# Performance work log

Measured on AMD Instinct MI355X. Metric: run time of the kernel, lower is better.

Reference implementation:

```python
import jax, jax.numpy as jnp
import numpy as np

N_GRAPHS = 8192
NODES_PER_GRAPH = 62
IN_CH = 4
HID = 64
NUM_CLASSES = 3
DEG = 8
N = N_GRAPHS * NODES_PER_GRAPH        # 507904 total nodes
E = N * DEG                            # 4063232 edges
BN_EPS = 1e-5


def setup_inputs() -> dict:
    key = jax.random.key(0)
    ks = jax.random.split(key, 24)

    def lin_w(k, i, o):
        return (jax.random.normal(k, (i, o), jnp.float32) / np.float32(np.sqrt(i)))

    inp = {
        "x": jax.random.normal(ks[0], (N, IN_CH), jnp.float32),
        "edge_src": jax.random.randint(ks[1], (E,), 0, N, dtype=jnp.int32),
        "edge_dst": jax.random.randint(ks[2], (E,), 0, N, dtype=jnp.int32),
        "num_graphs": N_GRAPHS,
        # conv1 MLP: Linear(4,64) -> ReLU -> Linear(64,64)
        "W1a": lin_w(ks[3], IN_CH, HID), "b1a": jnp.zeros((HID,), jnp.float32),
        "W1b": lin_w(ks[4], HID, HID),   "b1b": jnp.zeros((HID,), jnp.float32),
        "g1": jnp.ones((HID,), jnp.float32), "be1": jnp.zeros((HID,), jnp.float32),
        # conv2 MLP
        "W2a": lin_w(ks[5], HID, HID), "b2a": jnp.zeros((HID,), jnp.float32),
        "W2b": lin_w(ks[6], HID, HID), "b2b": jnp.zeros((HID,), jnp.float32),
        "g2": jnp.ones((HID,), jnp.float32), "be2": jnp.zeros((HID,), jnp.float32),
        # conv3 MLP
        "W3a": lin_w(ks[7], HID, HID), "b3a": jnp.zeros((HID,), jnp.float32),
        "W3b": lin_w(ks[8], HID, HID), "b3b": jnp.zeros((HID,), jnp.float32),
        "g3": jnp.ones((HID,), jnp.float32), "be3": jnp.zeros((HID,), jnp.float32),
        # final classifier fc2 (fc1 is unused in the original forward)
        "Wfc": lin_w(ks[9], HID, NUM_CLASSES), "bfc": jnp.zeros((NUM_CLASSES,), jnp.float32),
    }
    return inp


def _gin_conv(x, src, dst, Wa, ba, Wb, bb):
    # GINConv with eps=0: mlp(x_i + sum_{j->i} x_j)
    agg = jax.ops.segment_sum(x[src], dst, num_segments=N)
    h = x + agg
    return jnp.maximum(h @ Wa + ba, 0.0) @ Wb + bb


def _bn(h, g, b):
    # BatchNorm1d with batch statistics (training-mode math)
    m = h.mean(axis=0)
    v = h.var(axis=0)
    return (h - m) * jax.lax.rsqrt(v + BN_EPS) * g + b


def reference(x, edge_src, edge_dst, num_graphs,
              W1a, b1a, W1b, b1b, g1, be1,
              W2a, b2a, W2b, b2b, g2, be2,
              W3a, b3a, W3b, b3b, g3, be3,
              Wfc, bfc):
    h = _bn(jnp.maximum(_gin_conv(x, edge_src, edge_dst, W1a, b1a, W1b, b1b), 0.0), g1, be1)
    h = _bn(jnp.maximum(_gin_conv(h, edge_src, edge_dst, W2a, b2a, W2b, b2b), 0.0), g2, be2)
    h = _bn(jnp.maximum(_gin_conv(h, edge_src, edge_dst, W3a, b3a, W3b, b3b), 0.0), g3, be3)
    h = h.reshape(num_graphs, -1, HID).sum(axis=1)   # sum-pool nodes per graph
    # dropout is identity in eval mode
    return h @ Wfc + bfc
```

## Files before the change

kernel.cpp:

```cpp
#include <hip/hip_runtime.h>
#include <hip/hip_bf16.h>

#define NN   507904
#define NE   4063232
#define NG   8192
#define NPG  62
#define NBLKM 992

#define NB    248
#define BRNG  2048
#define BCAP  17152
#define PBCAP 31744
#define P3BLK 992
#define CSRSZ (NB * PBCAP)

#define OFF_R     0
#define OFF_AGGBF (OFF_R + NN * 64)
#define OFF_CSR   (OFF_AGGBF + NN * 32 + 32)
#define OFF_OC    (OFF_CSR + CSRSZ)
#define OFF_BCUR  (OFF_OC + 2 * NN)
#define OFF_PART  (OFF_BCUR + 256)
#define OFF_WTB   (OFF_PART + NBLKM * 128)
#define OFF_SS    (OFF_WTB + 11264)

#define WB_W1B 0
#define WB_W2A 4096
#define WB_W2B 8192
#define WB_W3A 12288
#define WB_W3B 16384
#define WB_W1A 20480

typedef __attribute__((ext_vector_type(8))) short short8;
typedef __attribute__((ext_vector_type(4))) float f32x4;
typedef unsigned short ushort_t;

__device__ __forceinline__ ushort_t f2bf_bits(float f) {
  union { float f; unsigned u; } x; x.f = f;
  unsigned r = x.u + 0x7FFF + ((x.u >> 16) & 1);
  return (ushort_t)(r >> 16);
}
__device__ __forceinline__ float bfu(ushort_t u) {
  union { unsigned i; float f; } x; x.i = ((unsigned)u) << 16; return x.f;
}

__global__ __launch_bounds__(256) void prep_weights(
    const float* __restrict__ w1a, const float* __restrict__ w1b,
    const float* __restrict__ w2a, const float* __restrict__ w2b,
    const float* __restrict__ w3a, const float* __restrict__ w3b,
    ushort_t* __restrict__ wtb, int* __restrict__ bcur,
    unsigned* __restrict__ sent1, unsigned* __restrict__ sent2) {
  int b = blockIdx.x, tid = threadIdx.x;
  if (b == 0) {
    ushort_t* d = wtb + WB_W1A;
    for (int i = tid; i < 2048; i += 256) {
      int n = i >> 5, k = i & 31;
      d[i] = (k < 4) ? f2bf_bits(w1a[k * 64 + n]) : (ushort_t)0;
    }
  } else if (b == 6) {
    bcur[tid] = 0;
    if (tid < 32) { sent1[tid] = 0; sent2[tid] = 0; }
  } else {
    const float* s; ushort_t* d;
    switch (b) {
      case 1: s = w1b; d = wtb + WB_W1B; break;
      case 2: s = w2a; d = wtb + WB_W2A; break;
      case 3: s = w2b; d = wtb + WB_W2B; break;
      case 4: s = w3a; d = wtb + WB_W3A; break;
      default: s = w3b; d = wtb + WB_W3B; break;
    }
    for (int i = tid; i < 4096; i += 256) {
      int k = i >> 6, n = i & 63;
      d[n * 64 + k] = f2bf_bits(s[i]);
    }
  }
}

__global__ __launch_bounds__(256) void p3_bin(
    const int* __restrict__ src, const int* __restrict__ dst,
    int* __restrict__ bcur, uint2* __restrict__ recs) {
  __shared__ int histo[256];
  __shared__ int scan_s[256];
  __shared__ int base_s[256];
  __shared__ int cur_s[256];
  __shared__ uint2 buf[4096];
  const int tid = threadIdx.x;
  const int e0 = blockIdx.x * 4096;

  histo[tid] = 0;
  __syncthreads();

  int d_[16], s_[16];
#pragma unroll
  for (int k = 0; k < 16; ++k) {
    int e = e0 + k * 256 + tid;
    d_[k] = dst[e]; s_[k] = src[e];
    atomicAdd(&histo[d_[k] >> 11], 1);
  }
  __syncthreads();

  int v = histo[tid];
  scan_s[tid] = v; __syncthreads();
  for (int s = 1; s < 256; s <<= 1) {
    int add = (tid >= s) ? scan_s[tid - s] : 0;
    __syncthreads();
    scan_s[tid] += add;
    __syncthreads();
  }
  int excl = scan_s[tid] - v;
  if (tid < NB) base_s[tid] = atomicAdd(&bcur[tid], v);
  cur_s[tid] = excl;
  histo[tid] = excl;
  __syncthreads();

#pragma unroll
  for (int k = 0; k < 16; ++k) {
    int b = d_[k] >> 11;
    int p = atomicAdd(&cur_s[b], 1);
    uint2 r; r.x = (unsigned)d_[k]; r.y = (unsigned)s_[k];
    buf[p] = r;
  }
  __syncthreads();

  for (int i = tid; i < 4096; i += 256) {
    uint2 r = buf[i];
    int b = (int)(r.x >> 11);
    int g = base_s[b] + (i - histo[b]);
    if (g < BCAP) recs[(size_t)b * BCAP + g] = r;
  }
}

__global__ __launch_bounds__(1024) void p4_build(
    const uint2* __restrict__ recs, const int* __restrict__ bcur,
    int* __restrict__ csr, int2* __restrict__ oc) {
  __shared__ int lcnt[2048];
  __shared__ int pscan[1024];
  __shared__ int sstart[2048];
  __shared__ int scur[2048];
  const int b = blockIdx.x, tid = threadIdx.x;
  int m = bcur[b]; if (m > BCAP) m = BCAP;
  const int cbase = b * PBCAP;
  const int nbase = b << 11;
  const uint2* rp = recs + (size_t)b * BCAP;

  lcnt[tid] = 0; lcnt[1024 + tid] = 0;
  __syncthreads();
  for (int i = tid; i < m; i += 1024)
    atomicAdd(&lcnt[rp[i].x & (BRNG - 1)], 1);
  __syncthreads();

  int a0 = lcnt[2 * tid], a1 = lcnt[2 * tid + 1];
  int p0 = (a0 + 7) & ~7, p1 = (a1 + 7) & ~7;
  int ps = p0 + p1;
  pscan[tid] = ps; __syncthreads();
  for (int s = 1; s < 1024; s <<= 1) {
    int add = (tid >= s) ? pscan[tid - s] : 0;
    __syncthreads();
    pscan[tid] += add;
    __syncthreads();
  }
  int e0 = pscan[tid] - ps;
  sstart[2 * tid] = e0;          scur[2 * tid] = e0;
  sstart[2 * tid + 1] = e0 + p0; scur[2 * tid + 1] = e0 + p0;
  __syncthreads();

  {
    int2 r0; r0.x = cbase + sstart[tid];        r0.y = lcnt[tid];
    int2 r1; r1.x = cbase + sstart[1024 + tid]; r1.y = lcnt[1024 + tid];
    oc[nbase + tid] = r0;
    oc[nbase + 1024 + tid] = r1;
  }
  __syncthreads();

  for (int i = tid; i < m; i += 1024) {
    uint2 r = rp[i];
    int p = atomicAdd(&scur[r.x & (BRNG - 1)], 1);
    csr[cbase + p] = (int)r.y;
  }
  __syncthreads();

#pragma unroll
  for (int k = 0; k < 2; ++k) {
    int i = k * 1024 + tid;
    int st = sstart[i], d = lcnt[i], p = (d + 7) & ~7;
    for (int q = d; q < p; ++q) csr[cbase + st + q] = NN;
  }
}

__global__ __launch_bounds__(256) void gather1(
    const float4* __restrict__ x, const int* __restrict__ csr,
    const int2* __restrict__ oc, float4* __restrict__ tout) {
  int n = blockIdx.x * 256 + threadIdx.x;
  float4 a = x[n];
  int2 oc_ = oc[n];
  int off = oc_.x, deg = oc_.y;
  const int* cp = csr + off;
  int j = 0;
  for (; j + 4 <= deg; j += 4) {
    int s0 = cp[j], s1 = cp[j + 1], s2 = cp[j + 2], s3 = cp[j + 3];
    float4 v0 = x[s0], v1 = x[s1], v2 = x[s2], v3 = x[s3];
    a.x += v0.x + v1.x + v2.x + v3.x;
    a.y += v0.y + v1.y + v2.y + v3.y;
    a.z += v0.z + v1.z + v2.z + v3.z;
    a.w += v0.w + v1.w + v2.w + v3.w;
  }
  for (; j < deg; ++j) {
    float4 v = x[cp[j]];
    a.x += v.x; a.y += v.y; a.z += v.z; a.w += v.w;
  }
  tout[n] = a;
}

template <bool L1, bool BFOUT>
__global__ __launch_bounds__(256) void mlp_mfma(
    const void* __restrict__ tin,
    const ushort_t* __restrict__ WaTb,
    const float* __restrict__ ba,
    const ushort_t* __restrict__ WbTb,
    const float* __restrict__ bb,
    float* __restrict__ routf, ushort_t* __restrict__ routb,
    float* __restrict__ part) {
  __shared__ __align__(16) ushort_t zt[4096];
  __shared__ float red[512];
  const int tid = threadIdx.x;
  const int wave = tid >> 6, lane = tid & 63;
  const int col = lane & 15, quad = lane >> 4;

  short8 bWa1[4];
  short8 bWa[2][4];
  short8 bWb[2][4];
#pragma unroll
  for (int nt = 0; nt < 4; ++nt) {
    if (L1) {
      bWa1[nt] = *(const short8*)(WaTb + (nt * 16 + col) * 32 + quad * 8);
    } else {
#pragma unroll
      for (int k0 = 0; k0 < 2; ++k0)
        bWa[k0][nt] = *(const short8*)(WaTb + (nt * 16 + col) * 64 + k0 * 32 + quad * 8);
    }
#pragma unroll
    for (int k0 = 0; k0 < 2; ++k0)
      bWb[k0][nt] = *(const short8*)(WbTb + (nt * 16 + col) * 64 + k0 * 32 + quad * 8);
  }
  float ba_n[4], bb_n[4];
#pragma unroll
  for (int nt = 0; nt < 4; ++nt) {
    ba_n[nt] = ba[nt * 16 + col];
    bb_n[nt] = bb[nt * 16 + col];
  }

  const int wbase = wave * 1024;
  float scol[4] = {0, 0, 0, 0}, qcol[4] = {0, 0, 0, 0};

  for (int it = 0; it < 8; ++it) {
    const int tile = blockIdx.x * 512 + it * 64 + wave * 16;

    f32x4 acc1[4];
#pragma unroll
    for (int nt = 0; nt < 4; ++nt) acc1[nt] = (f32x4){0.f, 0.f, 0.f, 0.f};

    if constexpr (L1) {
      float4 t4 = ((const float4*)tin)[tile + col];
      short8 az = {0, 0, 0, 0, 0, 0, 0, 0};
      if (quad == 0) {
        az[0] = (short)f2bf_bits(t4.x);
        az[1] = (short)f2bf_bits(t4.y);
        az[2] = (short)f2bf_bits(t4.z);
        az[3] = (short)f2bf_bits(t4.w);
      }
#pragma unroll
      for (int nt = 0; nt < 4; ++nt)
        acc1[nt] = __builtin_amdgcn_mfma_f32_16x16x32_bf16(az, bWa1[nt], acc1[nt], 0, 0, 0);
    } else {
      const ushort_t* tb = (const ushort_t*)tin;
      short8 a0 = *(const short8*)(tb + (size_t)(tile + col) * 64 + quad * 8);
      short8 a1 = *(const short8*)(tb + (size_t)(tile + col) * 64 + 32 + quad * 8);
#pragma unroll
      for (int nt = 0; nt < 4; ++nt) {
        acc1[nt] = __builtin_amdgcn_mfma_f32_16x16x32_bf16(a0, bWa[0][nt], acc1[nt], 0, 0, 0);
        acc1[nt] = __builtin_amdgcn_mfma_f32_16x16x32_bf16(a1, bWa[1][nt], acc1[nt], 0, 0, 0);
      }
    }

#pragma unroll
    for (int nt = 0; nt < 4; ++nt) {
      int oblk = nt * 2 + (col >> 3);
#pragma unroll
      for (int r = 0; r < 4; ++r) {
        int row = quad * 4 + r;
        float z = fmaxf(acc1[nt][r] + ba_n[nt], 0.0f);
        zt[wbase + row * 64 + (((oblk ^ (row & 7)) << 3) | (col & 7))] = f2bf_bits(z);
      }
    }
    short8 az0 = *(const short8*)&zt[wbase + col * 64 + ((quad ^ (col & 7)) << 3)];
    short8 az1 = *(const short8*)&zt[wbase + col * 64 + (((4 + quad) ^ (col & 7)) << 3)];

    f32x4 acc2[4];
#pragma unroll
    for (int nt = 0; nt < 4; ++nt) acc2[nt] = (f32x4){0.f, 0.f, 0.f, 0.f};
#pragma unroll
    for (int nt = 0; nt < 4; ++nt) {
      acc2[nt] = __builtin_amdgcn_mfma_f32_16x16x32_bf16(az0, bWb[0][nt], acc2[nt], 0, 0, 0);
      acc2[nt] = __builtin_amdgcn_mfma_f32_16x16x32_bf16(az1, bWb[1][nt], acc2[nt], 0, 0, 0);
    }
#pragma unroll
    for (int nt = 0; nt < 4; ++nt) {
#pragma unroll
      for (int r = 0; r < 4; ++r) {
        int row = tile + quad * 4 + r;
        float v = fmaxf(acc2[nt][r] + bb_n[nt], 0.0f);
        if (BFOUT) routb[(size_t)row * 64 + nt * 16 + col] = f2bf_bits(v);
        else       routf[(size_t)row * 64 + nt * 16 + col] = v;
        scol[nt] += v; qcol[nt] += v * v;
      }
    }
  }

#pragma unroll
  for (int nt = 0; nt < 4; ++nt) {
    float s = scol[nt], q = qcol[nt];
    s += __shfl_xor(s, 16); s += __shfl_xor(s, 32);
    q += __shfl_xor(q, 16); q += __shfl_xor(q, 32);
    if (quad == 0) {
      red[wave * 128 + nt * 16 + col] = s;
      red[wave * 128 + 64 + nt * 16 + col] = q;
    }
  }
  __syncthreads();
  if (tid < 128)
    part[blockIdx.x * 128 + tid] =
        red[tid] + red[128 + tid] + red[256 + tid] + red[384 + tid];
}

template <bool BFOUT>
__global__ __launch_bounds__(256) void mlp_fused(
    const ushort_t* __restrict__ h,
    const int* __restrict__ csr, const int2* __restrict__ oc,
    const float* __restrict__ ss,
    const ushort_t* __restrict__ WaTb,
    const float* __restrict__ ba,
    const ushort_t* __restrict__ WbTb,
    const float* __restrict__ bb,
    float* __restrict__ routf, ushort_t* __restrict__ routb,
    float* __restrict__ part) {
  __shared__ __align__(16) ushort_t zt[4096];
  __shared__ float red[512];
  __shared__ float ssl[128];
  const int tid = threadIdx.x;
  const int wave = tid >> 6, lane = tid & 63;
  const int col = lane & 15, quad = lane >> 4;
  if (tid < 128) ssl[tid] = ss[tid];

  short8 bWa[2][4], bWb[2][4];
#pragma unroll
  for (int nt = 0; nt < 4; ++nt) {
#pragma unroll
    for (int k0 = 0; k0 < 2; ++k0) {
      bWa[k0][nt] = *(const short8*)(WaTb + (nt * 16 + col) * 64 + k0 * 32 + quad * 8);
      bWb[k0][nt] = *(const short8*)(WbTb + (nt * 16 + col) * 64 + k0 * 32 + quad * 8);
    }
  }
  float ba_n[4], bb_n[4];
#pragma unroll
  for (int nt = 0; nt < 4; ++nt) {
    ba_n[nt] = ba[nt * 16 + col];
    bb_n[nt] = bb[nt * 16 + col];
  }
  __syncthreads();

  const float* scA = ssl + quad * 8;
  const float* scB = ssl + 32 + quad * 8;
  const float* sfA = ssl + 64 + quad * 8;
  const float* sfB = ssl + 96 + quad * 8;

  const int wbase = wave * 1024;
  float scol[4] = {0, 0, 0, 0}, qcol[4] = {0, 0, 0, 0};

  for (int it = 0; it < 8; ++it) {
    const int tile = blockIdx.x * 512 + it * 64 + wave * 16;
    const int row = tile + col;
    const int2 o = oc[row];

    const ushort_t* hp = h + (size_t)(unsigned)row * 64u + quad * 8;
    short8 sl0 = *(const short8*)hp;
    short8 sl1 = *(const short8*)(hp + 32);
    float accA[8], accB[8];
#pragma unroll
    for (int e = 0; e < 8; ++e) {
      accA[e] = bfu((ushort_t)sl0[e]);
      accB[e] = bfu((ushort_t)sl1[e]);
    }

    const int chunks = (o.y + 7) >> 3;
    for (int c = 0; c < chunks; ++c) {
      const int* cp = csr + o.x + (c << 3);
      int4 i0 = *(const int4*)cp;
      int4 i1 = *(const int4*)(cp + 4);
      int idx[8] = {i0.x, i0.y, i0.z, i0.w, i1.x, i1.y, i1.z, i1.w};
#pragma unroll
      for (int j = 0; j < 8; ++j) {
        const ushort_t* p = h + (size_t)(unsigned)idx[j] * 64u + quad * 8;
        short8 l0 = *(const short8*)p;
        short8 l1 = *(const short8*)(p + 32);
#pragma unroll
        for (int e = 0; e < 8; ++e) {
          accA[e] += bfu((ushort_t)l0[e]);
          accB[e] += bfu((ushort_t)l1[e]);
        }
      }
    }

    const float m1 = (float)(o.y + 1);
    short8 a0, a1;
#pragma unroll
    for (int e = 0; e < 8; ++e) {
      a0[e] = (short)f2bf_bits(fmaf(scA[e], accA[e], m1 * sfA[e]));
      a1[e] = (short)f2bf_bits(fmaf(scB[e], accB[e], m1 * sfB[e]));
    }

    f32x4 acc1[4];
#pragma unroll
    for (int nt = 0; nt < 4; ++nt) acc1[nt] = (f32x4){0.f, 0.f, 0.f, 0.f};
#pragma unroll
    for (int nt = 0; nt < 4; ++nt) {
      acc1[nt] = __builtin_amdgcn_mfma_f32_16x16x32_bf16(a0, bWa[0][nt], acc1[nt], 0, 0, 0);
      acc1[nt] = __builtin_amdgcn_mfma_f32_16x16x32_bf16(a1, bWa[1][nt], acc1[nt], 0, 0, 0);
    }

#pragma unroll
    for (int nt = 0; nt < 4; ++nt) {
      int oblk = nt * 2 + (col >> 3);
#pragma unroll
      for (int r = 0; r < 4; ++r) {
        int rw = quad * 4 + r;
        float z = fmaxf(acc1[nt][r] + ba_n[nt], 0.0f);
        zt[wbase + rw * 64 + (((oblk ^ (rw & 7)) << 3) | (col & 7))] = f2bf_bits(z);
      }
    }
    short8 az0 = *(const short8*)&zt[wbase + col * 64 + ((quad ^ (col & 7)) << 3)];
    short8 az1 = *(const short8*)&zt[wbase + col * 64 + (((4 + quad) ^ (col & 7)) << 3)];

    f32x4 acc2[4];
#pragma unroll
    for (int nt = 0; nt < 4; ++nt) acc2[nt] = (f32x4){0.f, 0.f, 0.f, 0.f};
#pragma unroll
    for (int nt = 0; nt < 4; ++nt) {
      acc2[nt] = __builtin_amdgcn_mfma_f32_16x16x32_bf16(az0, bWb[0][nt], acc2[nt], 0, 0, 0);
      acc2[nt] = __builtin_amdgcn_mfma_f32_16x16x32_bf16(az1, bWb[1][nt], acc2[nt], 0, 0, 0);
    }
#pragma unroll
    for (int nt = 0; nt < 4; ++nt) {
#pragma unroll
      for (int r = 0; r < 4; ++r) {
        int rw = tile + quad * 4 + r;
        float v = fmaxf(acc2[nt][r] + bb_n[nt], 0.0f);
        if (BFOUT) routb[(size_t)rw * 64 + nt * 16 + col] = f2bf_bits(v);
        else       routf[(size_t)rw * 64 + nt * 16 + col] = v;
        scol[nt] += v; qcol[nt] += v * v;
      }
    }
  }

#pragma unroll
  for (int nt = 0; nt < 4; ++nt) {
    float s = scol[nt], q = qcol[nt];
    s += __shfl_xor(s, 16); s += __shfl_xor(s, 32);
    q += __shfl_xor(q, 16); q += __shfl_xor(q, 32);
    if (quad == 0) {
      red[wave * 128 + nt * 16 + col] = s;
      red[wave * 128 + 64 + nt * 16 + col] = q;
    }
  }
  __syncthreads();
  if (tid < 128)
    part[blockIdx.x * 128 + tid] =
        red[tid] + red[128 + tid] + red[256 + tid] + red[384 + tid];
}

__global__ __launch_bounds__(256) void reduce_finalize(
    const float* __restrict__ part, const float* __restrict__ gma,
    const float* __restrict__ bta, float* __restrict__ ss) {
  __shared__ double sh[512];
  const int c = blockIdx.x, tid = threadIdx.x;
  double a = 0.0, b = 0.0;
  for (int blk = tid; blk < NBLKM; blk += 256) {
    a += (double)part[blk * 128 + c];
    b += (double)part[blk * 128 + 64 + c];
  }
  sh[tid] = a; sh[256 + tid] = b;
  __syncthreads();
  for (int s = 128; s; s >>= 1) {
    if (tid < s) { sh[tid] += sh[tid + s]; sh[256 + tid] += sh[256 + tid + s]; }
    __syncthreads();
  }
  if (tid == 0) {
    double mean = sh[0] / (double)NN;
    double var = sh[256] / (double)NN - mean * mean;
    double sc = (double)gma[c] / sqrt(var + 1e-5);
    ss[c] = (float)sc;
    ss[64 + c] = (float)((double)bta[c] - mean * sc);
  }
}

__global__ __launch_bounds__(64) void pool_fc(
    const float* __restrict__ r3, const float* __restrict__ ss,
    const float* __restrict__ wfc, const float* __restrict__ bfc,
    float* __restrict__ out) {
  int g = blockIdx.x, c = threadIdx.x;
  const float* base = r3 + (size_t)g * NPG * 64;
  float s = 0.f;
#pragma unroll
  for (int n = 0; n < NPG; ++n) s += base[n * 64 + c];
  float pooled = fmaf(ss[c], s, (float)NPG * ss[64 + c]);
#pragma unroll
  for (int j = 0; j < 3; ++j) {
    float v = pooled * wfc[c * 3 + j];
    for (int m = 32; m; m >>= 1) v += __shfl_xor(v, m);
    if (c == 0) out[g * 3 + j] = v + bfc[j];
  }
}

extern "C" void kernel_launch(void* const* d_in, const int* in_sizes, int n_in,
                              void* d_out, int out_size, void* d_ws, size_t ws_size,
                              hipStream_t stream) {
  const float* x    = (const float*)d_in[0];
  const int*   srcE = (const int*)d_in[1];
  const int*   dstE = (const int*)d_in[2];
  const float* W1a = (const float*)d_in[4],  *b1a = (const float*)d_in[5];
  const float* W1b = (const float*)d_in[6],  *b1b = (const float*)d_in[7];
  const float* g1  = (const float*)d_in[8],  *be1 = (const float*)d_in[9];
  const float* W2a = (const float*)d_in[10], *b2a = (const float*)d_in[11];
  const float* W2b = (const float*)d_in[12], *b2b = (const float*)d_in[13];
  const float* g2  = (const float*)d_in[14], *be2 = (const float*)d_in[15];
  const float* W3a = (const float*)d_in[16], *b3a = (const float*)d_in[17];
  const float* W3b = (const float*)d_in[18], *b3b = (const float*)d_in[19];
  const float* g3  = (const float*)d_in[20], *be3 = (const float*)d_in[21];
  const float* Wfc = (const float*)d_in[22], *bfc = (const float*)d_in[23];

  float* ws = (float*)d_ws;
  ushort_t* Rb     = (ushort_t*)(ws + OFF_R);
  float*    Rf     = ws + OFF_R;
  ushort_t* Ab     = (ushort_t*)(ws + OFF_AGGBF);
  void*     T1     = (void*)(ws + OFF_AGGBF);
  uint2*    RECS   = (uint2*)(ws + OFF_AGGBF);
  int*      CSR    = (int*)(ws + OFF_CSR);
  int2*     OC     = (int2*)(ws + OFF_OC);
  int*      BCUR   = (int*)(ws + OFF_BCUR);
  float*    PART   = ws + OFF_PART;
  ushort_t* WTB    = (ushort_t*)(ws + OFF_WTB);
  float*    SS     = ws + OFF_SS;

  prep_weights<<<7, 256, 0, stream>>>(W1a, W1b, W2a, W2b, W3a, W3b, WTB, BCUR,
                                      (unsigned*)(Rb + (size_t)NN * 64),
                                      (unsigned*)(Ab + (size_t)NN * 64));

  p3_bin<<<P3BLK, 256, 0, stream>>>(srcE, dstE, BCUR, RECS);
  p4_build<<<NB, 1024, 0, stream>>>(RECS, BCUR, CSR, OC);

  gather1<<<NN / 256, 256, 0, stream>>>((const float4*)x, CSR, OC, (float4*)T1);
  mlp_mfma<true, true><<<NBLKM, 256, 0, stream>>>(T1, WTB + WB_W1A, b1a,
                                                  WTB + WB_W1B, b1b,
                                                  nullptr, Rb, PART);
  reduce_finalize<<<64, 256, 0, stream>>>(PART, g1, be1, SS + 0);

  mlp_fused<true><<<NBLKM, 256, 0, stream>>>(Rb, CSR, OC, SS + 0,
                                             WTB + WB_W2A, b2a,
                                             WTB + WB_W2B, b2b,
                                             nullptr, Ab, PART);
  reduce_finalize<<<64, 256, 0, stream>>>(PART, g2, be2, SS + 128);

  mlp_fused<false><<<NBLKM, 256, 0, stream>>>(Ab, CSR, OC, SS + 128,
                                              WTB + WB_W3A, b3a,
                                              WTB + WB_W3B, b3b,
                                              Rf, nullptr, PART);
  reduce_finalize<<<64, 256, 0, stream>>>(PART, g3, be3, SS + 256);

  pool_fc<<<NG, 64, 0, stream>>>(Rf, SS + 256, Wfc, bfc, (float*)d_out);
}
```

Before: 567.8 us.

## Fuse graph sum-pooling into layer-3 MLP and coalesce bf16 output stores

Layer 3 no longer writes its full fp32 activation matrix. Each block accumulates per-graph sums in shared memory with atomics and flushes them to a global per-graph buffer with atomics, and a small fc_out kernel reads these sums. Layer 1 and layer 2 outputs are staged through swizzled LDS so each lane writes 16-byte vectors instead of scattered 2-byte stores. Blocks are halved in size, doubling the grid and the partial-stats count. The goal is to remove the large fp32 write and re-read for pooling and to improve store coalescing, at the cost of shared and global atomic contention.

```diff
diff --git a/kernel.cpp b/kernel.cpp
--- a/kernel.cpp
+++ b/kernel.cpp
@@ -5,7 +5,7 @@
 #define NE   4063232
 #define NG   8192
 #define NPG  62
-#define NBLKM 992
+#define NPBLK 1984
 
 #define NB    248
 #define BRNG  2048
@@ -15,12 +15,13 @@
 #define CSRSZ (NB * PBCAP)
 
 #define OFF_R     0
+#define OFF_GSUM  (OFF_R + NN * 32 + 64)
+#define OFF_PART  (OFF_GSUM + NG * 64)
 #define OFF_AGGBF (OFF_R + NN * 64)
 #define OFF_CSR   (OFF_AGGBF + NN * 32 + 32)
 #define OFF_OC    (OFF_CSR + CSRSZ)
 #define OFF_BCUR  (OFF_OC + 2 * NN)
-#define OFF_PART  (OFF_BCUR + 256)
-#define OFF_WTB   (OFF_PART + NBLKM * 128)
+#define OFF_WTB   (OFF_BCUR + 256)
 #define OFF_SS    (OFF_WTB + 11264)
 
 #define WB_W1B 0
@@ -48,7 +49,8 @@
     const float* __restrict__ w2a, const float* __restrict__ w2b,
     const float* __restrict__ w3a, const float* __restrict__ w3b,
     ushort_t* __restrict__ wtb, int* __restrict__ bcur,
-    unsigned* __restrict__ sent1, unsigned* __restrict__ sent2) {
+    unsigned* __restrict__ sent1, unsigned* __restrict__ sent2,
+    float* __restrict__ gsum) {
   int b = blockIdx.x, tid = threadIdx.x;
   if (b == 0) {
     ushort_t* d = wtb + WB_W1A;
@@ -59,6 +61,10 @@
   } else if (b == 6) {
     bcur[tid] = 0;
     if (tid < 32) { sent1[tid] = 0; sent2[tid] = 0; }
+  } else if (b >= 7) {
+    float* g = gsum + (size_t)(b - 7) * 1024;
+#pragma unroll
+    for (int k = 0; k < 4; ++k) g[k * 256 + tid] = 0.0f;
   } else {
     const float* s; ushort_t* d;
     switch (b) {
@@ -210,14 +216,13 @@
   tout[n] = a;
 }
 
-template <bool L1, bool BFOUT>
-__global__ __launch_bounds__(256) void mlp_mfma(
-    const void* __restrict__ tin,
+__global__ __launch_bounds__(256) void mlp_l1(
+    const float4* __restrict__ tin,
     const ushort_t* __restrict__ WaTb,
     const float* __restrict__ ba,
     const ushort_t* __restrict__ WbTb,
     const float* __restrict__ bb,
-    float* __restrict__ routf, ushort_t* __restrict__ routb,
+    ushort_t* __restrict__ routb,
     float* __restrict__ part) {
   __shared__ __align__(16) ushort_t zt[4096];
   __shared__ float red[512];
@@ -225,18 +230,10 @@
   const int wave = tid >> 6, lane = tid & 63;
   const int col = lane & 15, quad = lane >> 4;
 
-  short8 bWa1[4];
-  short8 bWa[2][4];
-  short8 bWb[2][4];
+  short8 bWa1[4], bWb[2][4];
 #pragma unroll
   for (int nt = 0; nt < 4; ++nt) {
-    if (L1) {
-      bWa1[nt] = *(const short8*)(WaTb + (nt * 16 + col) * 32 + quad * 8);
-    } else {
-#pragma unroll
-      for (int k0 = 0; k0 < 2; ++k0)
-        bWa[k0][nt] = *(const short8*)(WaTb + (nt * 16 + col) * 64 + k0 * 32 + quad * 8);
-    }
+    bWa1[nt] = *(const short8*)(WaTb + (nt * 16 + col) * 32 + quad * 8);
 #pragma unroll
     for (int k0 = 0; k0 < 2; ++k0)
       bWb[k0][nt] = *(const short8*)(WbTb + (nt * 16 + col) * 64 + k0 * 32 + quad * 8);
@@ -251,35 +248,24 @@
   const int wbase = wave * 1024;
   float scol[4] = {0, 0, 0, 0}, qcol[4] = {0, 0, 0, 0};
 
-  for (int it = 0; it < 8; ++it) {
-    const int tile = blockIdx.x * 512 + it * 64 + wave * 16;
+  for (int it = 0; it < 4; ++it) {
+    const int tile = blockIdx.x * 256 + it * 64 + wave * 16;
 
     f32x4 acc1[4];
 #pragma unroll
     for (int nt = 0; nt < 4; ++nt) acc1[nt] = (f32x4){0.f, 0.f, 0.f, 0.f};
 
-    if constexpr (L1) {
-      float4 t4 = ((const float4*)tin)[tile + col];
-      short8 az = {0, 0, 0, 0, 0, 0, 0, 0};
-      if (quad == 0) {
-        az[0] = (short)f2bf_bits(t4.x);
-        az[1] = (short)f2bf_bits(t4.y);
-        az[2] = (short)f2bf_bits(t4.z);
-        az[3] = (short)f2bf_bits(t4.w);
-      }
-#pragma unroll
-      for (int nt = 0; nt < 4; ++nt)
-        acc1[nt] = __builtin_amdgcn_mfma_f32_16x16x32_bf16(az, bWa1[nt], acc1[nt], 0, 0, 0);
-    } else {
-      const ushort_t* tb = (const ushort_t*)tin;
-      short8 a0 = *(const short8*)(tb + (size_t)(tile + col) * 64 + quad * 8);
-      short8 a1 = *(const short8*)(tb + (size_t)(tile + col) * 64 + 32 + quad * 8);
-#pragma unroll
-      for (int nt = 0; nt < 4; ++nt) {
-        acc1[nt] = __builtin_amdgcn_mfma_f32_16x16x32_bf16(a0, bWa[0][nt], acc1[nt], 0, 0, 0);
-        acc1[nt] = __builtin_amdgcn_mfma_f32_16x16x32_bf16(a1, bWa[1][nt], acc1[nt], 0, 0, 0);
-      }
-    }
+    float4 t4 = tin[tile + col];
+    short8 az = {0, 0, 0, 0, 0, 0, 0, 0};
+    if (quad == 0) {
+      az[0] = (short)f2bf_bits(t4.x);
+      az[1] = (short)f2bf_bits(t4.y);
+      az[2] = (short)f2bf_bits(t4.z);
+      az[3] = (short)f2bf_bits(t4.w);
+    }
+#pragma unroll
+    for (int nt = 0; nt < 4; ++nt)
+      acc1[nt] = __builtin_amdgcn_mfma_f32_16x16x32_bf16(az, bWa1[nt], acc1[nt], 0, 0, 0);
 
 #pragma unroll
     for (int nt = 0; nt < 4; ++nt) {
@@ -304,14 +290,22 @@
     }
 #pragma unroll
     for (int nt = 0; nt < 4; ++nt) {
+      int oblk = nt * 2 + (col >> 3);
 #pragma unroll
       for (int r = 0; r < 4; ++r) {
-        int row = tile + quad * 4 + r;
+        int rw = quad * 4 + r;
         float v = fmaxf(acc2[nt][r] + bb_n[nt], 0.0f);
-        if (BFOUT) routb[(size_t)row * 64 + nt * 16 + col] = f2bf_bits(v);
-        else       routf[(size_t)row * 64 + nt * 16 + col] = v;
+        zt[wbase + rw * 64 + (((oblk ^ (rw & 7)) << 3) | (col & 7))] = f2bf_bits(v);
         scol[nt] += v; qcol[nt] += v * v;
       }
+    }
+    {
+      const int R = lane >> 2, sp = lane & 3;
+      short8 w0 = *(const short8*)&zt[wbase + R * 64 + (((sp * 2) ^ (R & 7)) << 3)];
+      short8 w1 = *(const short8*)&zt[wbase + R * 64 + (((sp * 2 + 1) ^ (R & 7)) << 3)];
+      ushort_t* dst = routb + (size_t)(tile + R) * 64 + sp * 16;
+      *(short8*)dst = w0;
+      *(short8*)(dst + 8) = w1;
     }
   }
 
@@ -331,7 +325,7 @@
         red[tid] + red[128 + tid] + red[256 + tid] + red[384 + tid];
 }
 
-template <bool BFOUT>
+template <bool GS>
 __global__ __launch_bounds__(256) void mlp_fused(
     const ushort_t* __restrict__ h,
     const int* __restrict__ csr, const int2* __restrict__ oc,
@@ -340,15 +334,20 @@
     const float* __restrict__ ba,
     const ushort_t* __restrict__ WbTb,
     const float* __restrict__ bb,
-    float* __restrict__ routf, ushort_t* __restrict__ routb,
+    ushort_t* __restrict__ routb, float* __restrict__ gsum_g,
     float* __restrict__ part) {
   __shared__ __align__(16) ushort_t zt[4096];
   __shared__ float red[512];
   __shared__ float ssl[128];
+  __shared__ float gsum[GS ? 384 : 1];
   const int tid = threadIdx.x;
   const int wave = tid >> 6, lane = tid & 63;
   const int col = lane & 15, quad = lane >> 4;
   if (tid < 128) ssl[tid] = ss[tid];
+  const int g0 = (blockIdx.x * 256) / 62;
+  if (GS) {
+    for (int i = tid; i < 384; i += 256) gsum[i] = 0.0f;
+  }
 
   short8 bWa[2][4], bWb[2][4];
 #pragma unroll
@@ -375,8 +374,8 @@
   const int wbase = wave * 1024;
   float scol[4] = {0, 0, 0, 0}, qcol[4] = {0, 0, 0, 0};
 
-  for (int it = 0; it < 8; ++it) {
-    const int tile = blockIdx.x * 512 + it * 64 + wave * 16;
+  for (int it = 0; it < 4; ++it) {
+    const int tile = blockIdx.x * 256 + it * 64 + wave * 16;
     const int row = tile + col;
     const int2 o = oc[row];
 
@@ -447,16 +446,37 @@
       acc2[nt] = __builtin_amdgcn_mfma_f32_16x16x32_bf16(az0, bWb[0][nt], acc2[nt], 0, 0, 0);
       acc2[nt] = __builtin_amdgcn_mfma_f32_16x16x32_bf16(az1, bWb[1][nt], acc2[nt], 0, 0, 0);
     }
-#pragma unroll
-    for (int nt = 0; nt < 4; ++nt) {
-#pragma unroll
-      for (int r = 0; r < 4; ++r) {
-        int rw = tile + quad * 4 + r;
-        float v = fmaxf(acc2[nt][r] + bb_n[nt], 0.0f);
-        if (BFOUT) routb[(size_t)rw * 64 + nt * 16 + col] = f2bf_bits(v);
-        else       routf[(size_t)rw * 64 + nt * 16 + col] = v;
-        scol[nt] += v; qcol[nt] += v * v;
+
+    if (GS) {
+#pragma unroll
+      for (int nt = 0; nt < 4; ++nt) {
+#pragma unroll
+        for (int r = 0; r < 4; ++r) {
+          int rw = tile + quad * 4 + r;
+          float v = fmaxf(acc2[nt][r] + bb_n[nt], 0.0f);
+          scol[nt] += v; qcol[nt] += v * v;
+          int gl = rw / 62 - g0;
+          atomicAdd(&gsum[gl * 64 + nt * 16 + col], v);
+        }
       }
+    } else {
+#pragma unroll
+      for (int nt = 0; nt < 4; ++nt) {
+        int oblk = nt * 2 + (col >> 3);
+#pragma unroll
+        for (int r = 0; r < 4; ++r) {
+          int rw = quad * 4 + r;
+          float v = fmaxf(acc2[nt][r] + bb_n[nt], 0.0f);
+          zt[wbase + rw * 64 + (((oblk ^ (rw & 7)) << 3) | (col & 7))] = f2bf_bits(v);
+          scol[nt] += v; qcol[nt] += v * v;
+        }
+      }
+      const int R = lane >> 2, sp = lane & 3;
+      short8 w0 = *(const short8*)&zt[wbase + R * 64 + (((sp * 2) ^ (R & 7)) << 3)];
+      short8 w1 = *(const short8*)&zt[wbase + R * 64 + (((sp * 2 + 1) ^ (R & 7)) << 3)];
+      ushort_t* dst = routb + (size_t)(tile + R) * 64 + sp * 16;
+      *(short8*)dst = w0;
+      *(short8*)(dst + 8) = w1;
     }
   }
 
@@ -474,6 +494,14 @@
   if (tid < 128)
     part[blockIdx.x * 128 + tid] =
         red[tid] + red[128 + tid] + red[256 + tid] + red[384 + tid];
+
+  if (GS) {
+    for (int i = tid; i < 384; i += 256) {
+      int g = g0 + (i >> 6);
+      float v = gsum[i];
+      if (g < NG && v != 0.0f) atomicAdd(&gsum_g[(size_t)g * 64 + (i & 63)], v);
+    }
+  }
 }
 
 __global__ __launch_bounds__(256) void reduce_finalize(
@@ -482,7 +510,7 @@
   __shared__ double sh[512];
   const int c = blockIdx.x, tid = threadIdx.x;
   double a = 0.0, b = 0.0;
-  for (int blk = tid; blk < NBLKM; blk += 256) {
+  for (int blk = tid; blk < NPBLK; blk += 256) {
     a += (double)part[blk * 128 + c];
     b += (double)part[blk * 128 + 64 + c];
   }
@@ -501,15 +529,14 @@
   }
 }
 
-__global__ __launch_bounds__(64) void pool_fc(
-    const float* __restrict__ r3, const float* __restrict__ ss,
+__global__ __launch_bounds__(256) void fc_out(
+    const float* __restrict__ gsum_g, const float* __restrict__ ss,
     const float* __restrict__ wfc, const float* __restrict__ bfc,
     float* __restrict__ out) {
-  int g = blockIdx.x, c = threadIdx.x;
-  const float* base = r3 + (size_t)g * NPG * 64;
-  float s = 0.f;
-#pragma unroll
-  for (int n = 0; n < NPG; ++n) s += base[n * 64 + c];
+  const int lane = threadIdx.x & 63;
+  const int g = blockIdx.x * 4 + (threadIdx.x >> 6);
+  const int c = lane;
+  float s = gsum_g[(size_t)g * 64 + c];
   float pooled = fmaf(ss[c], s, (float)NPG * ss[64 + c]);
 #pragma unroll
   for (int j = 0; j < 3; ++j) {
@@ -538,41 +565,41 @@
 
   float* ws = (float*)d_ws;
   ushort_t* Rb     = (ushort_t*)(ws + OFF_R);
-  float*    Rf     = ws + OFF_R;
+  float*    GSUM   = ws + OFF_GSUM;
+  float*    PART   = ws + OFF_PART;
   ushort_t* Ab     = (ushort_t*)(ws + OFF_AGGBF);
   void*     T1     = (void*)(ws + OFF_AGGBF);
   uint2*    RECS   = (uint2*)(ws + OFF_AGGBF);
   int*      CSR    = (int*)(ws + OFF_CSR);
   int2*     OC     = (int2*)(ws + OFF_OC);
   int*      BCUR   = (int*)(ws + OFF_BCUR);
-  float*    PART   = ws + OFF_PART;
   ushort_t* WTB    = (ushort_t*)(ws + OFF_WTB);
   float*    SS     = ws + OFF_SS;
 
-  prep_weights<<<7, 256, 0, stream>>>(W1a, W1b, W2a, W2b, W3a, W3b, WTB, BCUR,
-                                      (unsigned*)(Rb + (size_t)NN * 64),
-                                      (unsigned*)(Ab + (size_t)NN * 64));
+  prep_weights<<<519, 256, 0, stream>>>(W1a, W1b, W2a, W2b, W3a, W3b, WTB, BCUR,
+                                        (unsigned*)(Rb + (size_t)NN * 64),
+                                        (unsigned*)(Ab + (size_t)NN * 64),
+                                        GSUM);
 
   p3_bin<<<P3BLK, 256, 0, stream>>>(srcE, dstE, BCUR, RECS);
   p4_build<<<NB, 1024, 0, stream>>>(RECS, BCUR, CSR, OC);
 
   gather1<<<NN / 256, 256, 0, stream>>>((const float4*)x, CSR, OC, (float4*)T1);
-  mlp_mfma<true, true><<<NBLKM, 256, 0, stream>>>(T1, WTB + WB_W1A, b1a,
-                                                  WTB + WB_W1B, b1b,
-                                                  nullptr, Rb, PART);
+  mlp_l1<<<NPBLK, 256, 0, stream>>>((const float4*)T1, WTB + WB_W1A, b1a,
+                                    WTB + WB_W1B, b1b, Rb, PART);
   reduce_finalize<<<64, 256, 0, stream>>>(PART, g1, be1, SS + 0);
 
-  mlp_fused<true><<<NBLKM, 256, 0, stream>>>(Rb, CSR, OC, SS + 0,
-                                             WTB + WB_W2A, b2a,
-                                             WTB + WB_W2B, b2b,
-                                             nullptr, Ab, PART);
+  mlp_fused<false><<<NPBLK, 256, 0, stream>>>(Rb, CSR, OC, SS + 0,
+                                              WTB + WB_W2A, b2a,
+                                              WTB + WB_W2B, b2b,
+                                              Ab, nullptr, PART);
   reduce_finalize<<<64, 256, 0, stream>>>(PART, g2, be2, SS + 128);
 
-  mlp_fused<false><<<NBLKM, 256, 0, stream>>>(Ab, CSR, OC, SS + 128,
-                                              WTB + WB_W3A, b3a,
-                                              WTB + WB_W3B, b3b,
-                                              Rf, nullptr, PART);
+  mlp_fused<true><<<NPBLK, 256, 0, stream>>>(Ab, CSR, OC, SS + 128,
+                                             WTB + WB_W3A, b3a,
+                                             WTB + WB_W3B, b3b,
+                                             nullptr, GSUM, PART);
   reduce_finalize<<<64, 256, 0, stream>>>(PART, g3, be3, SS + 256);
 
-  pool_fc<<<NG, 64, 0, stream>>>(Rf, SS + 256, Wfc, bfc, (float*)d_out);
-}
+  fc_out<<<NG / 4, 256, 0, stream>>>(GSUM, SS + 256, Wfc, bfc, (float*)d_out);
+}
```

Result: slower. 646.5 us (+13.9%).
